# Kernel optimization log

Measured on AMD Instinct MI355X. Metric: run time of the kernel, lower is better.

## Reference

```python
import jax, jax.numpy as jnp
import numpy as np

MAX_ABS = 1.0          # assumed get_max_abs('T')
DT = 0.01              # forward default dt
TWO_PI = 2.0 * np.pi
B, D, N = 4096, 2048, 4096


def setup_inputs() -> dict:
    key = jax.random.key(0)
    k0, k1 = jax.random.split(key, 2)
    x = jax.random.normal(k0, (B, D), dtype=jnp.float32)
    # nn.Linear params
    W = jax.random.normal(k1, (N, D), dtype=jnp.float32) * (1.0 / np.sqrt(D))
    b = jnp.zeros((N,), dtype=jnp.float32)
    # oscillator params (as initialized in __init__)
    amplitude = jnp.ones((N,), dtype=jnp.float32)
    frequency = jnp.ones((N,), dtype=jnp.float32)
    phase_offset = jnp.zeros((N,), dtype=jnp.float32)
    damping = jnp.full((N,), 0.01, dtype=jnp.float32)
    return {"x": x, "W": W, "b": b, "amplitude": amplitude,
            "frequency": frequency, "phase_offset": phase_offset,
            "damping": damping}


def reference(x, W, b, amplitude, frequency, phase_offset, damping):
    # driving force: [B, N]
    force = x @ W.T + b
    omega_sq = (TWO_PI * frequency) ** 2  # [N]
    # t starts at 0 and is incremented ONCE per forward call
    t = DT

    def step(carry, f):
        state, vel = carry
        accel = -omega_sq * state - damping * vel + f
        vel = vel + accel * DT
        state = state + vel * DT
        return (state, vel), state

    init = (jnp.zeros((N,), x.dtype), jnp.zeros((N,), x.dtype))
    (_, _), states = jax.lax.scan(step, init, force)  # states: [B, N]

    # sinusoid term is identical for every batch step (t fixed within forward)
    osc = amplitude * jnp.sin(TWO_PI * frequency * t + phase_offset)  # [N]
    out = jnp.clip(states + osc, -MAX_ABS, MAX_ABS)
    return out
```

## Files before the change

### kernel.cpp

```cpp
#include <hip/hip_runtime.h>
#include <hip/hip_bf16.h>
#include <math.h>

#define MDIM 4096
#define KDIM 2048
#define NDIM 4096
#define DT   0.01f
#define TWO_PI_F 6.283185307179586f
#define CH 64
#define CL 64

typedef __attribute__((ext_vector_type(8))) short bf16x8;
typedef __attribute__((ext_vector_type(4))) float f32x4;

__device__ __forceinline__ unsigned short f2bf(float f) {
  unsigned int u = __float_as_uint(f);
  u += 0x7FFFu + ((u >> 16) & 1u);
  return (unsigned short)(u >> 16);
}
__device__ __forceinline__ float bf2f(unsigned short u) {
  return __uint_as_float(((unsigned int)u) << 16);
}

__global__ void cast_bf16_kernel(const float* __restrict__ src,
                                 unsigned short* __restrict__ dst, int n4) {
  int i = blockIdx.x * blockDim.x + threadIdx.x;
  if (i >= n4) return;
  float4 v = ((const float4*)src)[i];
  ushort4 o;
  o.x = f2bf(v.x); o.y = f2bf(v.y); o.z = f2bf(v.z); o.w = f2bf(v.w);
  ((ushort4*)dst)[i] = o;
}

__global__ __launch_bounds__(256, 2) void gemm_bt_kernel(
    const unsigned short* __restrict__ A,
    const unsigned short* __restrict__ Bm,
    const float* __restrict__ bias,
    unsigned short* __restrict__ C) {
  __shared__ __align__(16) unsigned short sA[128 * 32];
  __shared__ __align__(16) unsigned short sB[128 * 32];

  const int tid  = threadIdx.x;
  const int lane = tid & 63;
  const int wave = tid >> 6;
  const int wr = wave >> 1;
  const int wc = wave & 1;
  const int q  = lane >> 4;
  const int lm = lane & 15;

  const int bM = blockIdx.x * 128;
  const int bN = blockIdx.y * 128;

  f32x4 acc[4][4];
#pragma unroll
  for (int i = 0; i < 4; i++)
#pragma unroll
    for (int j = 0; j < 4; j++) acc[i][j] = (f32x4){0.f, 0.f, 0.f, 0.f};

  const int idx0 = tid;
  const int idx1 = tid + 256;
  const int r0 = idx0 >> 2, c0 = (idx0 & 3) * 8;
  const int r1 = idx1 >> 2, c1 = (idx1 & 3) * 8;

  for (int k0 = 0; k0 < KDIM; k0 += 32) {
    uint4 av0 = *(const uint4*)&A [(size_t)(bM + r0) * KDIM + k0 + c0];
    uint4 av1 = *(const uint4*)&A [(size_t)(bM + r1) * KDIM + k0 + c1];
    uint4 bv0 = *(const uint4*)&Bm[(size_t)(bN + r0) * KDIM + k0 + c0];
    uint4 bv1 = *(const uint4*)&Bm[(size_t)(bN + r1) * KDIM + k0 + c1];
    __syncthreads();
    *(uint4*)&sA[idx0 * 8] = av0;
    *(uint4*)&sA[idx1 * 8] = av1;
    *(uint4*)&sB[idx0 * 8] = bv0;
    *(uint4*)&sB[idx1 * 8] = bv1;
    __syncthreads();

    bf16x8 af[4], bfr[4];
#pragma unroll
    for (int mt = 0; mt < 4; mt++)
      af[mt]  = *(const bf16x8*)&sA[(wr * 64 + mt * 16 + lm) * 32 + q * 8];
#pragma unroll
    for (int nt = 0; nt < 4; nt++)
      bfr[nt] = *(const bf16x8*)&sB[(wc * 64 + nt * 16 + lm) * 32 + q * 8];

#pragma unroll
    for (int mt = 0; mt < 4; mt++)
#pragma unroll
      for (int nt = 0; nt < 4; nt++)
        acc[mt][nt] = __builtin_amdgcn_mfma_f32_16x16x32_bf16(
            af[mt], bfr[nt], acc[mt][nt], 0, 0, 0);
  }

#pragma unroll
  for (int nt = 0; nt < 4; nt++) {
    const int col = bN + wc * 64 + nt * 16 + lm;
    const float bz = bias[col];
#pragma unroll
    for (int mt = 0; mt < 4; mt++) {
      const int row0 = bM + wr * 64 + mt * 16 + q * 4;
#pragma unroll
      for (int r = 0; r < 4; r++)
        C[(size_t)(row0 + r) * NDIM + col] = f2bf(acc[mt][nt][r] + bz);
    }
  }
}

__global__ void scan_pass1(const unsigned short* __restrict__ force,
                           const float* __restrict__ freq,
                           const float* __restrict__ damp,
                           float* __restrict__ chunkS,
                           float* __restrict__ chunkV) {
  int gid = blockIdx.x * blockDim.x + threadIdx.x;
  int n = gid & (NDIM - 1);
  int c = gid >> 12;
  float om = TWO_PI_F * freq[n];
  float osq = om * om;
  float dp = damp[n];
  float s = 0.f, v = 0.f;
  const unsigned short* fp = force + (size_t)c * CL * NDIM + n;
#pragma unroll 8
  for (int i = 0; i < CL; i++) {
    float f = bf2f(fp[(size_t)i * NDIM]);
    float a = -osq * s - dp * v + f;
    v += a * DT;
    s += v * DT;
  }
  chunkS[gid] = s;
  chunkV[gid] = v;
}

__global__ void scan_pass2(const float* __restrict__ chunkS,
                           const float* __restrict__ chunkV,
                           const float* __restrict__ freq,
                           const float* __restrict__ damp,
                           float* __restrict__ carryS,
                           float* __restrict__ carryV) {
  int n = blockIdx.x * blockDim.x + threadIdx.x;
  float om = TWO_PI_F * freq[n];
  float osq = om * om;
  float dp = damp[n];
  float a00 = 1.f - osq * DT * DT, a01 = DT * (1.f - dp * DT);
  float a10 = -osq * DT,           a11 = 1.f - dp * DT;
#pragma unroll
  for (int i = 0; i < 6; i++) {
    float b00 = a00 * a00 + a01 * a10;
    float b01 = a00 * a01 + a01 * a11;
    float b10 = a10 * a00 + a11 * a10;
    float b11 = a10 * a01 + a11 * a11;
    a00 = b00; a01 = b01; a10 = b10; a11 = b11;
  }
  float cs = 0.f, cv = 0.f;
#pragma unroll 8
  for (int c = 0; c < CH; c++) {
    carryS[c * NDIM + n] = cs;
    carryV[c * NDIM + n] = cv;
    float ls = chunkS[c * NDIM + n];
    float lv = chunkV[c * NDIM + n];
    float ns = a00 * cs + a01 * cv + ls;
    float nv = a10 * cs + a11 * cv + lv;
    cs = ns; cv = nv;
  }
}

__global__ void scan_pass3(const unsigned short* __restrict__ force,
                           const float* __restrict__ amp,
                           const float* __restrict__ freq,
                           const float* __restrict__ phase,
                           const float* __restrict__ damp,
                           const float* __restrict__ carryS,
                           const float* __restrict__ carryV,
                           float* __restrict__ out) {
  int gid = blockIdx.x * blockDim.x + threadIdx.x;
  int n = gid & (NDIM - 1);
  int c = gid >> 12;
  float om = TWO_PI_F * freq[n];
  float osq = om * om;
  float dp = damp[n];
  float osc = amp[n] * sinf(om * DT + phase[n]);
  float s = carryS[gid], v = carryV[gid];
  const unsigned short* fp = force + (size_t)c * CL * NDIM + n;
  float* op = out + (size_t)c * CL * NDIM + n;
#pragma unroll 8
  for (int i = 0; i < CL; i++) {
    float f = bf2f(fp[(size_t)i * NDIM]);
    float a = -osq * s - dp * v + f;
    v += a * DT;
    s += v * DT;
    float o = s + osc;
    o = fminf(1.f, fmaxf(-1.f, o));
    op[(size_t)i * NDIM] = o;
  }
}

extern "C" void kernel_launch(void* const* d_in, const int* in_sizes, int n_in,
                              void* d_out, int out_size, void* d_ws, size_t ws_size,
                              hipStream_t stream) {
  const float* x     = (const float*)d_in[0];
  const float* W     = (const float*)d_in[1];
  const float* bias  = (const float*)d_in[2];
  const float* amp   = (const float*)d_in[3];
  const float* freq  = (const float*)d_in[4];
  const float* phase = (const float*)d_in[5];
  const float* damp  = (const float*)d_in[6];

  unsigned short* xbf   = (unsigned short*)d_ws;
  unsigned short* wbf   = xbf + (size_t)MDIM * KDIM;
  unsigned short* force = wbf + (size_t)NDIM * KDIM;
  float* chunkS = (float*)d_ws;
  float* chunkV = chunkS + CH * NDIM;
  float* carryS = chunkV + CH * NDIM;
  float* carryV = carryS + CH * NDIM;

  cast_bf16_kernel<<<(MDIM * KDIM / 4 + 255) / 256, 256, 0, stream>>>(
      x, xbf, MDIM * KDIM / 4);
  cast_bf16_kernel<<<(NDIM * KDIM / 4 + 255) / 256, 256, 0, stream>>>(
      W, wbf, NDIM * KDIM / 4);

  dim3 gg(MDIM / 128, NDIM / 128);
  gemm_bt_kernel<<<gg, 256, 0, stream>>>(xbf, wbf, bias, force);

  scan_pass1<<<CH * NDIM / 256, 256, 0, stream>>>(force, freq, damp,
                                                  chunkS, chunkV);
  scan_pass2<<<NDIM / 256, 256, 0, stream>>>(chunkS, chunkV, freq, damp,
                                             carryS, carryV);
  scan_pass3<<<CH * NDIM / 256, 256, 0, stream>>>(
      force, amp, freq, phase, damp, carryS, carryV, (float*)d_out);
}
```

Baseline: 235.3 us.

## Use direct global-to-LDS loads in GEMM, vectorize scans, merge cast kernels

```diff
diff --git a/kernel.cpp b/kernel.cpp
--- a/kernel.cpp
+++ b/kernel.cpp
@@ -13,6 +13,11 @@
 typedef __attribute__((ext_vector_type(8))) short bf16x8;
 typedef __attribute__((ext_vector_type(4))) float f32x4;
 
+#define GLD_LDS16(g, l)                                             \
+  __builtin_amdgcn_global_load_lds(                                 \
+      (const __attribute__((address_space(1))) unsigned int*)(g),   \
+      (__attribute__((address_space(3))) unsigned int*)(l), 16, 0, 0)
+
 __device__ __forceinline__ unsigned short f2bf(float f) {
   unsigned int u = __float_as_uint(f);
   u += 0x7FFFu + ((u >> 16) & 1u);
@@ -22,14 +27,21 @@
   return __uint_as_float(((unsigned int)u) << 16);
 }
 
-__global__ void cast_bf16_kernel(const float* __restrict__ src,
-                                 unsigned short* __restrict__ dst, int n4) {
+__global__ void cast2_bf16_kernel(const float* __restrict__ s0,
+                                  unsigned short* __restrict__ d0,
+                                  const float* __restrict__ s1,
+                                  unsigned short* __restrict__ d1,
+                                  int n4each) {
   int i = blockIdx.x * blockDim.x + threadIdx.x;
-  if (i >= n4) return;
-  float4 v = ((const float4*)src)[i];
+  const float4* sp;
+  ushort4* dp;
+  int j;
+  if (i < n4each) { sp = (const float4*)s0; dp = (ushort4*)d0; j = i; }
+  else            { sp = (const float4*)s1; dp = (ushort4*)d1; j = i - n4each; }
+  float4 v = sp[j];
   ushort4 o;
   o.x = f2bf(v.x); o.y = f2bf(v.y); o.z = f2bf(v.z); o.w = f2bf(v.w);
-  ((ushort4*)dst)[i] = o;
+  dp[j] = o;
 }
 
 __global__ __launch_bounds__(256, 2) void gemm_bt_kernel(
@@ -61,17 +73,17 @@
   const int idx1 = tid + 256;
   const int r0 = idx0 >> 2, c0 = (idx0 & 3) * 8;
   const int r1 = idx1 >> 2, c1 = (idx1 & 3) * 8;
+  const unsigned short* gA0 = A  + (size_t)(bM + r0) * KDIM + c0;
+  const unsigned short* gA1 = A  + (size_t)(bM + r1) * KDIM + c1;
+  const unsigned short* gB0 = Bm + (size_t)(bN + r0) * KDIM + c0;
+  const unsigned short* gB1 = Bm + (size_t)(bN + r1) * KDIM + c1;
 
   for (int k0 = 0; k0 < KDIM; k0 += 32) {
-    uint4 av0 = *(const uint4*)&A [(size_t)(bM + r0) * KDIM + k0 + c0];
-    uint4 av1 = *(const uint4*)&A [(size_t)(bM + r1) * KDIM + k0 + c1];
-    uint4 bv0 = *(const uint4*)&Bm[(size_t)(bN + r0) * KDIM + k0 + c0];
-    uint4 bv1 = *(const uint4*)&Bm[(size_t)(bN + r1) * KDIM + k0 + c1];
     __syncthreads();
-    *(uint4*)&sA[idx0 * 8] = av0;
-    *(uint4*)&sA[idx1 * 8] = av1;
-    *(uint4*)&sB[idx0 * 8] = bv0;
-    *(uint4*)&sB[idx1 * 8] = bv1;
+    GLD_LDS16(gA0 + k0, &sA[idx0 * 8]);
+    GLD_LDS16(gA1 + k0, &sA[idx1 * 8]);
+    GLD_LDS16(gB0 + k0, &sB[idx0 * 8]);
+    GLD_LDS16(gB1 + k0, &sB[idx1 * 8]);
     __syncthreads();
 
     bf16x8 af[4], bfr[4];
@@ -110,22 +122,30 @@
                            float* __restrict__ chunkS,
                            float* __restrict__ chunkV) {
   int gid = blockIdx.x * blockDim.x + threadIdx.x;
-  int n = gid & (NDIM - 1);
-  int c = gid >> 12;
-  float om = TWO_PI_F * freq[n];
-  float osq = om * om;
-  float dp = damp[n];
-  float s = 0.f, v = 0.f;
+  int n4 = gid & (NDIM / 4 - 1);
+  int c  = gid >> 10;
+  int n  = n4 * 4;
+  float4 fr = *(const float4*)&freq[n];
+  float4 dv = *(const float4*)&damp[n];
+  float osq[4] = {TWO_PI_F * fr.x, TWO_PI_F * fr.y, TWO_PI_F * fr.z, TWO_PI_F * fr.w};
+  float dp[4]  = {dv.x, dv.y, dv.z, dv.w};
+  float s[4] = {0.f, 0.f, 0.f, 0.f}, v[4] = {0.f, 0.f, 0.f, 0.f};
+#pragma unroll
+  for (int j = 0; j < 4; j++) osq[j] *= osq[j];
   const unsigned short* fp = force + (size_t)c * CL * NDIM + n;
-#pragma unroll 8
+#pragma unroll 4
   for (int i = 0; i < CL; i++) {
-    float f = bf2f(fp[(size_t)i * NDIM]);
-    float a = -osq * s - dp * v + f;
-    v += a * DT;
-    s += v * DT;
-  }
-  chunkS[gid] = s;
-  chunkV[gid] = v;
+    ushort4 fv = *(const ushort4*)&fp[(size_t)i * NDIM];
+    float f[4] = {bf2f(fv.x), bf2f(fv.y), bf2f(fv.z), bf2f(fv.w)};
+#pragma unroll
+    for (int j = 0; j < 4; j++) {
+      float a = -osq[j] * s[j] - dp[j] * v[j] + f[j];
+      v[j] += a * DT;
+      s[j] += v[j] * DT;
+    }
+  }
+  *(float4*)&chunkS[c * NDIM + n] = (float4){s[0], s[1], s[2], s[3]};
+  *(float4*)&chunkV[c * NDIM + n] = (float4){v[0], v[1], v[2], v[3]};
 }
 
 __global__ void scan_pass2(const float* __restrict__ chunkS,
@@ -170,24 +190,42 @@
                            const float* __restrict__ carryV,
                            float* __restrict__ out) {
   int gid = blockIdx.x * blockDim.x + threadIdx.x;
-  int n = gid & (NDIM - 1);
-  int c = gid >> 12;
-  float om = TWO_PI_F * freq[n];
-  float osq = om * om;
-  float dp = damp[n];
-  float osc = amp[n] * sinf(om * DT + phase[n]);
-  float s = carryS[gid], v = carryV[gid];
+  int n4 = gid & (NDIM / 4 - 1);
+  int c  = gid >> 10;
+  int n  = n4 * 4;
+  float4 fr = *(const float4*)&freq[n];
+  float4 dv = *(const float4*)&damp[n];
+  float4 am = *(const float4*)&amp[n];
+  float4 ph = *(const float4*)&phase[n];
+  float om[4] = {TWO_PI_F * fr.x, TWO_PI_F * fr.y, TWO_PI_F * fr.z, TWO_PI_F * fr.w};
+  float dp[4] = {dv.x, dv.y, dv.z, dv.w};
+  float osq[4], osc[4], s[4], v[4];
+  float amv[4] = {am.x, am.y, am.z, am.w};
+  float phv[4] = {ph.x, ph.y, ph.z, ph.w};
+#pragma unroll
+  for (int j = 0; j < 4; j++) {
+    osq[j] = om[j] * om[j];
+    osc[j] = amv[j] * sinf(om[j] * DT + phv[j]);
+  }
+  float4 csv = *(const float4*)&carryS[c * NDIM + n];
+  float4 cvv = *(const float4*)&carryV[c * NDIM + n];
+  s[0] = csv.x; s[1] = csv.y; s[2] = csv.z; s[3] = csv.w;
+  v[0] = cvv.x; v[1] = cvv.y; v[2] = cvv.z; v[3] = cvv.w;
   const unsigned short* fp = force + (size_t)c * CL * NDIM + n;
   float* op = out + (size_t)c * CL * NDIM + n;
-#pragma unroll 8
+#pragma unroll 4
   for (int i = 0; i < CL; i++) {
-    float f = bf2f(fp[(size_t)i * NDIM]);
-    float a = -osq * s - dp * v + f;
-    v += a * DT;
-    s += v * DT;
-    float o = s + osc;
-    o = fminf(1.f, fmaxf(-1.f, o));
-    op[(size_t)i * NDIM] = o;
+    ushort4 fv = *(const ushort4*)&fp[(size_t)i * NDIM];
+    float f[4] = {bf2f(fv.x), bf2f(fv.y), bf2f(fv.z), bf2f(fv.w)};
+    float o[4];
+#pragma unroll
+    for (int j = 0; j < 4; j++) {
+      float a = -osq[j] * s[j] - dp[j] * v[j] + f[j];
+      v[j] += a * DT;
+      s[j] += v[j] * DT;
+      o[j] = fminf(1.f, fmaxf(-1.f, s[j] + osc[j]));
+    }
+    *(float4*)&op[(size_t)i * NDIM] = (float4){o[0], o[1], o[2], o[3]};
   }
 }
 
@@ -210,18 +248,17 @@
   float* carryS = chunkV + CH * NDIM;
   float* carryV = carryS + CH * NDIM;
 
-  cast_bf16_kernel<<<(MDIM * KDIM / 4 + 255) / 256, 256, 0, stream>>>(
-      x, xbf, MDIM * KDIM / 4);
-  cast_bf16_kernel<<<(NDIM * KDIM / 4 + 255) / 256, 256, 0, stream>>>(
-      W, wbf, NDIM * KDIM / 4);
+  const int n4each = MDIM * KDIM / 4;
+  cast2_bf16_kernel<<<(2 * n4each + 255) / 256, 256, 0, stream>>>(
+      x, xbf, W, wbf, n4each);
 
   dim3 gg(MDIM / 128, NDIM / 128);
   gemm_bt_kernel<<<gg, 256, 0, stream>>>(xbf, wbf, bias, force);
 
-  scan_pass1<<<CH * NDIM / 256, 256, 0, stream>>>(force, freq, damp,
-                                                  chunkS, chunkV);
+  scan_pass1<<<CH * NDIM / 4 / 256, 256, 0, stream>>>(force, freq, damp,
+                                                      chunkS, chunkV);
   scan_pass2<<<NDIM / 256, 256, 0, stream>>>(chunkS, chunkV, freq, damp,
                                              carryS, carryV);
-  scan_pass3<<<CH * NDIM / 256, 256, 0, stream>>>(
+  scan_pass3<<<CH * NDIM / 4 / 256, 256, 0, stream>>>(
       force, amp, freq, phase, damp, carryS, carryV, (float*)d_out);
 }
```

After: 231.4 us. Within noise of the previous version (-1.6%).

## Fuse three-pass oscillator scan into one cooperative kernel with LDS-cached force

Applied to the files above, without the earlier changes.

```diff
diff --git a/kernel.cpp b/kernel.cpp
--- a/kernel.cpp
+++ b/kernel.cpp
@@ -1,6 +1,9 @@
 #include <hip/hip_runtime.h>
 #include <hip/hip_bf16.h>
+#include <hip/hip_cooperative_groups.h>
 #include <math.h>
+
+namespace cg = cooperative_groups;
 
 #define MDIM 4096
 #define KDIM 2048
@@ -22,14 +25,21 @@
   return __uint_as_float(((unsigned int)u) << 16);
 }
 
-__global__ void cast_bf16_kernel(const float* __restrict__ src,
-                                 unsigned short* __restrict__ dst, int n4) {
+__global__ void cast2_bf16_kernel(const float* __restrict__ s0,
+                                  unsigned short* __restrict__ d0,
+                                  const float* __restrict__ s1,
+                                  unsigned short* __restrict__ d1,
+                                  int n4each) {
   int i = blockIdx.x * blockDim.x + threadIdx.x;
-  if (i >= n4) return;
-  float4 v = ((const float4*)src)[i];
+  const float4* sp;
+  ushort4* dp;
+  int j;
+  if (i < n4each) { sp = (const float4*)s0; dp = (ushort4*)d0; j = i; }
+  else            { sp = (const float4*)s1; dp = (ushort4*)d1; j = i - n4each; }
+  float4 v = sp[j];
   ushort4 o;
   o.x = f2bf(v.x); o.y = f2bf(v.y); o.z = f2bf(v.z); o.w = f2bf(v.w);
-  ((ushort4*)dst)[i] = o;
+  dp[j] = o;
 }
 
 __global__ __launch_bounds__(256, 2) void gemm_bt_kernel(
@@ -104,90 +114,89 @@
   }
 }
 
-__global__ void scan_pass1(const unsigned short* __restrict__ force,
-                           const float* __restrict__ freq,
-                           const float* __restrict__ damp,
-                           float* __restrict__ chunkS,
-                           float* __restrict__ chunkV) {
-  int gid = blockIdx.x * blockDim.x + threadIdx.x;
-  int n = gid & (NDIM - 1);
-  int c = gid >> 12;
-  float om = TWO_PI_F * freq[n];
-  float osq = om * om;
-  float dp = damp[n];
-  float s = 0.f, v = 0.f;
-  const unsigned short* fp = force + (size_t)c * CL * NDIM + n;
+__global__ __launch_bounds__(256, 2) void scan_fused(
+    const unsigned short* __restrict__ force,
+    const float* __restrict__ amp,
+    const float* __restrict__ freq,
+    const float* __restrict__ phase,
+    const float* __restrict__ damp,
+    float* __restrict__ chunkS,
+    float* __restrict__ chunkV,
+    float* __restrict__ out) {
+  __shared__ __align__(16) unsigned short sF[CL * 512];
+
+  const int tid = threadIdx.x;
+  const int c = blockIdx.x >> 3;
+  const int colBase = (blockIdx.x & 7) * 512;
+
+#pragma unroll
+  for (int k = 0; k < 16; k++) {
+    int slot = tid + 256 * k;
+    *(uint4*)&sF[slot * 8] =
+        *(const uint4*)&force[((size_t)c * CL + (slot >> 6)) * NDIM +
+                              colBase + (slot & 63) * 8];
+  }
+  __syncthreads();
+
+  const int n = colBase + tid * 2;
+  float2 fr = *(const float2*)&freq[n];
+  float2 dv = *(const float2*)&damp[n];
+  const float om0 = TWO_PI_F * fr.x, om1 = TWO_PI_F * fr.y;
+  const float osq0 = om0 * om0,      osq1 = om1 * om1;
+  const float dp0 = dv.x,            dp1 = dv.y;
+
+  float s0 = 0.f, v0 = 0.f, s1 = 0.f, v1 = 0.f;
 #pragma unroll 8
   for (int i = 0; i < CL; i++) {
-    float f = bf2f(fp[(size_t)i * NDIM]);
-    float a = -osq * s - dp * v + f;
-    v += a * DT;
-    s += v * DT;
-  }
-  chunkS[gid] = s;
-  chunkV[gid] = v;
-}
-
-__global__ void scan_pass2(const float* __restrict__ chunkS,
-                           const float* __restrict__ chunkV,
-                           const float* __restrict__ freq,
-                           const float* __restrict__ damp,
-                           float* __restrict__ carryS,
-                           float* __restrict__ carryV) {
-  int n = blockIdx.x * blockDim.x + threadIdx.x;
-  float om = TWO_PI_F * freq[n];
-  float osq = om * om;
-  float dp = damp[n];
-  float a00 = 1.f - osq * DT * DT, a01 = DT * (1.f - dp * DT);
-  float a10 = -osq * DT,           a11 = 1.f - dp * DT;
+    ushort2 f2 = *(const ushort2*)&sF[i * 512 + tid * 2];
+    float f0 = bf2f(f2.x), f1 = bf2f(f2.y);
+    v0 += (-osq0 * s0 - dp0 * v0 + f0) * DT;  s0 += v0 * DT;
+    v1 += (-osq1 * s1 - dp1 * v1 + f1) * DT;  s1 += v1 * DT;
+  }
+  *(float2*)&chunkS[c * NDIM + n] = make_float2(s0, s1);
+  *(float2*)&chunkV[c * NDIM + n] = make_float2(v0, v1);
+  __threadfence();
+  cg::this_grid().sync();
+
+  float p00 = 1.f - osq0 * DT * DT, p01 = DT * (1.f - dp0 * DT);
+  float p10 = -osq0 * DT,           p11 = 1.f - dp0 * DT;
+  float q00 = 1.f - osq1 * DT * DT, q01 = DT * (1.f - dp1 * DT);
+  float q10 = -osq1 * DT,           q11 = 1.f - dp1 * DT;
 #pragma unroll
   for (int i = 0; i < 6; i++) {
-    float b00 = a00 * a00 + a01 * a10;
-    float b01 = a00 * a01 + a01 * a11;
-    float b10 = a10 * a00 + a11 * a10;
-    float b11 = a10 * a01 + a11 * a11;
-    a00 = b00; a01 = b01; a10 = b10; a11 = b11;
-  }
-  float cs = 0.f, cv = 0.f;
-#pragma unroll 8
-  for (int c = 0; c < CH; c++) {
-    carryS[c * NDIM + n] = cs;
-    carryV[c * NDIM + n] = cv;
-    float ls = chunkS[c * NDIM + n];
-    float lv = chunkV[c * NDIM + n];
-    float ns = a00 * cs + a01 * cv + ls;
-    float nv = a10 * cs + a11 * cv + lv;
-    cs = ns; cv = nv;
-  }
-}
-
-__global__ void scan_pass3(const unsigned short* __restrict__ force,
-                           const float* __restrict__ amp,
-                           const float* __restrict__ freq,
-                           const float* __restrict__ phase,
-                           const float* __restrict__ damp,
-                           const float* __restrict__ carryS,
-                           const float* __restrict__ carryV,
-                           float* __restrict__ out) {
-  int gid = blockIdx.x * blockDim.x + threadIdx.x;
-  int n = gid & (NDIM - 1);
-  int c = gid >> 12;
-  float om = TWO_PI_F * freq[n];
-  float osq = om * om;
-  float dp = damp[n];
-  float osc = amp[n] * sinf(om * DT + phase[n]);
-  float s = carryS[gid], v = carryV[gid];
-  const unsigned short* fp = force + (size_t)c * CL * NDIM + n;
-  float* op = out + (size_t)c * CL * NDIM + n;
+    float b00 = p00 * p00 + p01 * p10, b01 = p00 * p01 + p01 * p11;
+    float b10 = p10 * p00 + p11 * p10, b11 = p10 * p01 + p11 * p11;
+    p00 = b00; p01 = b01; p10 = b10; p11 = b11;
+    float d00 = q00 * q00 + q01 * q10, d01 = q00 * q01 + q01 * q11;
+    float d10 = q10 * q00 + q11 * q10, d11 = q10 * q01 + q11 * q11;
+    q00 = d00; q01 = d01; q10 = d10; q11 = d11;
+  }
+  float cs0 = 0.f, cv0 = 0.f, cs1 = 0.f, cv1 = 0.f;
+  for (int cc = 0; cc < c; cc++) {
+    float2 ls = *(const float2*)&chunkS[cc * NDIM + n];
+    float2 lv = *(const float2*)&chunkV[cc * NDIM + n];
+    float t0 = p00 * cs0 + p01 * cv0 + ls.x;
+    float u0 = p10 * cs0 + p11 * cv0 + lv.x;
+    cs0 = t0; cv0 = u0;
+    float t1 = q00 * cs1 + q01 * cv1 + ls.y;
+    float u1 = q10 * cs1 + q11 * cv1 + lv.y;
+    cs1 = t1; cv1 = u1;
+  }
+
+  float2 am = *(const float2*)&amp[n];
+  float2 ph = *(const float2*)&phase[n];
+  const float osc0 = am.x * sinf(om0 * DT + ph.x);
+  const float osc1 = am.y * sinf(om1 * DT + ph.y);
+  s0 = cs0; v0 = cv0; s1 = cs1; v1 = cv1;
 #pragma unroll 8
   for (int i = 0; i < CL; i++) {
-    float f = bf2f(fp[(size_t)i * NDIM]);
-    float a = -osq * s - dp * v + f;
-    v += a * DT;
-    s += v * DT;
-    float o = s + osc;
-    o = fminf(1.f, fmaxf(-1.f, o));
-    op[(size_t)i * NDIM] = o;
+    ushort2 f2 = *(const ushort2*)&sF[i * 512 + tid * 2];
+    float f0 = bf2f(f2.x), f1 = bf2f(f2.y);
+    v0 += (-osq0 * s0 - dp0 * v0 + f0) * DT;  s0 += v0 * DT;
+    v1 += (-osq1 * s1 - dp1 * v1 + f1) * DT;  s1 += v1 * DT;
+    float o0 = fminf(1.f, fmaxf(-1.f, s0 + osc0));
+    float o1 = fminf(1.f, fmaxf(-1.f, s1 + osc1));
+    *(float2*)&out[((size_t)c * CL + i) * NDIM + n] = make_float2(o0, o1);
   }
 }
 
@@ -207,21 +216,17 @@
   unsigned short* force = wbf + (size_t)NDIM * KDIM;
   float* chunkS = (float*)d_ws;
   float* chunkV = chunkS + CH * NDIM;
-  float* carryS = chunkV + CH * NDIM;
-  float* carryV = carryS + CH * NDIM;
-
-  cast_bf16_kernel<<<(MDIM * KDIM / 4 + 255) / 256, 256, 0, stream>>>(
-      x, xbf, MDIM * KDIM / 4);
-  cast_bf16_kernel<<<(NDIM * KDIM / 4 + 255) / 256, 256, 0, stream>>>(
-      W, wbf, NDIM * KDIM / 4);
+  float* outp   = (float*)d_out;
+
+  const int n4each = MDIM * KDIM / 4;
+  cast2_bf16_kernel<<<(2 * n4each + 255) / 256, 256, 0, stream>>>(
+      x, xbf, W, wbf, n4each);
 
   dim3 gg(MDIM / 128, NDIM / 128);
   gemm_bt_kernel<<<gg, 256, 0, stream>>>(xbf, wbf, bias, force);
 
-  scan_pass1<<<CH * NDIM / 256, 256, 0, stream>>>(force, freq, damp,
-                                                  chunkS, chunkV);
-  scan_pass2<<<NDIM / 256, 256, 0, stream>>>(chunkS, chunkV, freq, damp,
-                                             carryS, carryV);
-  scan_pass3<<<CH * NDIM / 256, 256, 0, stream>>>(
-      force, amp, freq, phase, damp, carryS, carryV, (float*)d_out);
-}
+  void* args[] = {(void*)&force, (void*)&amp, (void*)&freq, (void*)&phase,
+                  (void*)&damp, (void*)&chunkS, (void*)&chunkV, (void*)&outp};
+  hipLaunchCooperativeKernel((const void*)scan_fused, dim3(CH * 8), dim3(256),
+                             args, 0, stream);
+}
```

Result: slower. 326.7 us (+38.9%).

## Fuse bf16 cast and local chunk scan into GEMM, merge carry and output passes

Applied to the files above, without the earlier changes.

```diff
diff --git a/kernel.cpp b/kernel.cpp
--- a/kernel.cpp
+++ b/kernel.cpp
@@ -21,24 +21,23 @@
 __device__ __forceinline__ float bf2f(unsigned short u) {
   return __uint_as_float(((unsigned int)u) << 16);
 }
-
-__global__ void cast_bf16_kernel(const float* __restrict__ src,
-                                 unsigned short* __restrict__ dst, int n4) {
-  int i = blockIdx.x * blockDim.x + threadIdx.x;
-  if (i >= n4) return;
-  float4 v = ((const float4*)src)[i];
-  ushort4 o;
-  o.x = f2bf(v.x); o.y = f2bf(v.y); o.z = f2bf(v.z); o.w = f2bf(v.w);
-  ((ushort4*)dst)[i] = o;
-}
-
-__global__ __launch_bounds__(256, 2) void gemm_bt_kernel(
-    const unsigned short* __restrict__ A,
-    const unsigned short* __restrict__ Bm,
+__device__ __forceinline__ unsigned int pk2(float lo, float hi) {
+  __hip_bfloat162 h = __float22bfloat162_rn(make_float2(lo, hi));
+  return *(unsigned int*)&h;
+}
+
+__global__ __launch_bounds__(256, 2) void gemm_scan_kernel(
+    const float* __restrict__ A,
+    const float* __restrict__ Bm,
     const float* __restrict__ bias,
-    unsigned short* __restrict__ C) {
-  __shared__ __align__(16) unsigned short sA[128 * 32];
-  __shared__ __align__(16) unsigned short sB[128 * 32];
+    const float* __restrict__ freq,
+    const float* __restrict__ damp,
+    unsigned short* __restrict__ zpart,
+    float* __restrict__ chunkS,
+    float* __restrict__ chunkV) {
+  __shared__ __align__(16) unsigned short smem[16384];
+  unsigned short* sA = smem;
+  unsigned short* sB = smem + 4096;
 
   const int tid  = threadIdx.x;
   const int lane = tid & 63;
@@ -61,12 +60,24 @@
   const int idx1 = tid + 256;
   const int r0 = idx0 >> 2, c0 = (idx0 & 3) * 8;
   const int r1 = idx1 >> 2, c1 = (idx1 & 3) * 8;
+  const float* gA0 = A  + (size_t)(bM + r0) * KDIM + c0;
+  const float* gA1 = A  + (size_t)(bM + r1) * KDIM + c1;
+  const float* gB0 = Bm + (size_t)(bN + r0) * KDIM + c0;
+  const float* gB1 = Bm + (size_t)(bN + r1) * KDIM + c1;
 
   for (int k0 = 0; k0 < KDIM; k0 += 32) {
-    uint4 av0 = *(const uint4*)&A [(size_t)(bM + r0) * KDIM + k0 + c0];
-    uint4 av1 = *(const uint4*)&A [(size_t)(bM + r1) * KDIM + k0 + c1];
-    uint4 bv0 = *(const uint4*)&Bm[(size_t)(bN + r0) * KDIM + k0 + c0];
-    uint4 bv1 = *(const uint4*)&Bm[(size_t)(bN + r1) * KDIM + k0 + c1];
+    float4 aL0 = *(const float4*)(gA0 + k0);
+    float4 aH0 = *(const float4*)(gA0 + k0 + 4);
+    float4 aL1 = *(const float4*)(gA1 + k0);
+    float4 aH1 = *(const float4*)(gA1 + k0 + 4);
+    float4 bL0 = *(const float4*)(gB0 + k0);
+    float4 bH0 = *(const float4*)(gB0 + k0 + 4);
+    float4 bL1 = *(const float4*)(gB1 + k0);
+    float4 bH1 = *(const float4*)(gB1 + k0 + 4);
+    uint4 av0 = {pk2(aL0.x,aL0.y), pk2(aL0.z,aL0.w), pk2(aH0.x,aH0.y), pk2(aH0.z,aH0.w)};
+    uint4 av1 = {pk2(aL1.x,aL1.y), pk2(aL1.z,aL1.w), pk2(aH1.x,aH1.y), pk2(aH1.z,aH1.w)};
+    uint4 bv0 = {pk2(bL0.x,bL0.y), pk2(bL0.z,bL0.w), pk2(bH0.x,bH0.y), pk2(bH0.z,bH0.w)};
+    uint4 bv1 = {pk2(bL1.x,bL1.y), pk2(bL1.z,bL1.w), pk2(bH1.x,bH1.y), pk2(bH1.z,bH1.w)};
     __syncthreads();
     *(uint4*)&sA[idx0 * 8] = av0;
     *(uint4*)&sA[idx1 * 8] = av1;
@@ -90,104 +101,119 @@
             af[mt], bfr[nt], acc[mt][nt], 0, 0, 0);
   }
 
+  __syncthreads();
+  unsigned short* sT = smem + wave * 4096;
 #pragma unroll
   for (int nt = 0; nt < 4; nt++) {
-    const int col = bN + wc * 64 + nt * 16 + lm;
-    const float bz = bias[col];
-#pragma unroll
-    for (int mt = 0; mt < 4; mt++) {
-      const int row0 = bM + wr * 64 + mt * 16 + q * 4;
+    const float bz = bias[bN + wc * 64 + nt * 16 + lm];
+#pragma unroll
+    for (int mt = 0; mt < 4; mt++)
 #pragma unroll
       for (int r = 0; r < 4; r++)
-        C[(size_t)(row0 + r) * NDIM + col] = f2bf(acc[mt][nt][r] + bz);
-    }
-  }
-}
-
-__global__ void scan_pass1(const unsigned short* __restrict__ force,
-                           const float* __restrict__ freq,
-                           const float* __restrict__ damp,
-                           float* __restrict__ chunkS,
-                           float* __restrict__ chunkV) {
-  int gid = blockIdx.x * blockDim.x + threadIdx.x;
-  int n = gid & (NDIM - 1);
-  int c = gid >> 12;
-  float om = TWO_PI_F * freq[n];
-  float osq = om * om;
-  float dp = damp[n];
+        sT[(mt * 16 + q * 4 + r) * 64 + nt * 16 + lm] =
+            f2bf(acc[mt][nt][r] + bz);
+  }
+  __syncthreads();
+
+  const int gcol = bN + wc * 64 + lane;
+  const float om  = TWO_PI_F * freq[gcol];
+  const float osq = om * om;
+  const float dp  = damp[gcol];
   float s = 0.f, v = 0.f;
-  const unsigned short* fp = force + (size_t)c * CL * NDIM + n;
 #pragma unroll 8
   for (int i = 0; i < CL; i++) {
-    float f = bf2f(fp[(size_t)i * NDIM]);
-    float a = -osq * s - dp * v + f;
-    v += a * DT;
+    float f = bf2f(sT[i * 64 + lane]);
+    v += (-osq * s - dp * v + f) * DT;
     s += v * DT;
-  }
-  chunkS[gid] = s;
-  chunkV[gid] = v;
-}
-
-__global__ void scan_pass2(const float* __restrict__ chunkS,
-                           const float* __restrict__ chunkV,
-                           const float* __restrict__ freq,
-                           const float* __restrict__ damp,
-                           float* __restrict__ carryS,
-                           float* __restrict__ carryV) {
-  int n = blockIdx.x * blockDim.x + threadIdx.x;
-  float om = TWO_PI_F * freq[n];
-  float osq = om * om;
-  float dp = damp[n];
-  float a00 = 1.f - osq * DT * DT, a01 = DT * (1.f - dp * DT);
-  float a10 = -osq * DT,           a11 = 1.f - dp * DT;
-#pragma unroll
-  for (int i = 0; i < 6; i++) {
-    float b00 = a00 * a00 + a01 * a10;
-    float b01 = a00 * a01 + a01 * a11;
-    float b10 = a10 * a00 + a11 * a10;
-    float b11 = a10 * a01 + a11 * a11;
-    a00 = b00; a01 = b01; a10 = b10; a11 = b11;
-  }
-  float cs = 0.f, cv = 0.f;
-#pragma unroll 8
-  for (int c = 0; c < CH; c++) {
-    carryS[c * NDIM + n] = cs;
-    carryV[c * NDIM + n] = cv;
-    float ls = chunkS[c * NDIM + n];
-    float lv = chunkV[c * NDIM + n];
-    float ns = a00 * cs + a01 * cv + ls;
-    float nv = a10 * cs + a11 * cv + lv;
-    cs = ns; cv = nv;
-  }
-}
-
-__global__ void scan_pass3(const unsigned short* __restrict__ force,
-                           const float* __restrict__ amp,
-                           const float* __restrict__ freq,
-                           const float* __restrict__ phase,
-                           const float* __restrict__ damp,
-                           const float* __restrict__ carryS,
-                           const float* __restrict__ carryV,
-                           float* __restrict__ out) {
+    sT[i * 64 + lane] = f2bf(s);
+  }
+  const int chunk = 2 * blockIdx.x + wr;
+  chunkS[chunk * NDIM + gcol] = s;
+  chunkV[chunk * NDIM + gcol] = v;
+  __syncthreads();
+
+#pragma unroll
+  for (int k = 0; k < 8; k++) {
+    int slot = lane + 64 * k;
+    int row  = slot >> 3;
+    int col8 = (slot & 7) * 8;
+    *(uint4*)&zpart[(size_t)(bM + wr * 64 + row) * NDIM + bN + wc * 64 + col8] =
+        *(uint4*)&sT[row * 64 + col8];
+  }
+}
+
+__global__ void scan_out_kernel(const unsigned short* __restrict__ zpart,
+                                const float* __restrict__ amp,
+                                const float* __restrict__ freq,
+                                const float* __restrict__ phase,
+                                const float* __restrict__ damp,
+                                const float* __restrict__ chunkS,
+                                const float* __restrict__ chunkV,
+                                float* __restrict__ out) {
   int gid = blockIdx.x * blockDim.x + threadIdx.x;
-  int n = gid & (NDIM - 1);
-  int c = gid >> 12;
-  float om = TWO_PI_F * freq[n];
-  float osq = om * om;
-  float dp = damp[n];
-  float osc = amp[n] * sinf(om * DT + phase[n]);
-  float s = carryS[gid], v = carryV[gid];
-  const unsigned short* fp = force + (size_t)c * CL * NDIM + n;
+  int n4 = gid & (NDIM / 4 - 1);
+  int c  = gid >> 10;
+  int n  = n4 * 4;
+
+  float4 fr = *(const float4*)&freq[n];
+  float4 dv = *(const float4*)&damp[n];
+  float4 am = *(const float4*)&amp[n];
+  float4 ph = *(const float4*)&phase[n];
+  float omv[4] = {TWO_PI_F * fr.x, TWO_PI_F * fr.y, TWO_PI_F * fr.z, TWO_PI_F * fr.w};
+  float dpv[4] = {dv.x, dv.y, dv.z, dv.w};
+  float amv[4] = {am.x, am.y, am.z, am.w};
+  float phv[4] = {ph.x, ph.y, ph.z, ph.w};
+  float m00[4], m01[4], m10[4], m11[4];
+  float p00[4], p01[4], p10[4], p11[4];
+  float osc[4];
+#pragma unroll
+  for (int j = 0; j < 4; j++) {
+    float osq = omv[j] * omv[j];
+    m00[j] = 1.f - osq * DT * DT;  m01[j] = DT * (1.f - dpv[j] * DT);
+    m10[j] = -osq * DT;            m11[j] = 1.f - dpv[j] * DT;
+    p00[j] = m00[j]; p01[j] = m01[j]; p10[j] = m10[j]; p11[j] = m11[j];
+    osc[j] = amv[j] * sinf(omv[j] * DT + phv[j]);
+  }
+#pragma unroll
+  for (int i = 0; i < 6; i++)
+#pragma unroll
+    for (int j = 0; j < 4; j++) {
+      float b00 = p00[j] * p00[j] + p01[j] * p10[j];
+      float b01 = p00[j] * p01[j] + p01[j] * p11[j];
+      float b10 = p10[j] * p00[j] + p11[j] * p10[j];
+      float b11 = p10[j] * p01[j] + p11[j] * p11[j];
+      p00[j] = b00; p01[j] = b01; p10[j] = b10; p11[j] = b11;
+    }
+
+  float hs[4] = {0.f, 0.f, 0.f, 0.f}, hv[4] = {0.f, 0.f, 0.f, 0.f};
+  for (int cc = 0; cc < c; cc++) {
+    float4 ls = *(const float4*)&chunkS[cc * NDIM + n];
+    float4 lv = *(const float4*)&chunkV[cc * NDIM + n];
+    float lsv[4] = {ls.x, ls.y, ls.z, ls.w};
+    float lvv[4] = {lv.x, lv.y, lv.z, lv.w};
+#pragma unroll
+    for (int j = 0; j < 4; j++) {
+      float t = p00[j] * hs[j] + p01[j] * hv[j] + lsv[j];
+      float u = p10[j] * hs[j] + p11[j] * hv[j] + lvv[j];
+      hs[j] = t; hv[j] = u;
+    }
+  }
+
+  const unsigned short* zp = zpart + (size_t)c * CL * NDIM + n;
   float* op = out + (size_t)c * CL * NDIM + n;
-#pragma unroll 8
+#pragma unroll 4
   for (int i = 0; i < CL; i++) {
-    float f = bf2f(fp[(size_t)i * NDIM]);
-    float a = -osq * s - dp * v + f;
-    v += a * DT;
-    s += v * DT;
-    float o = s + osc;
-    o = fminf(1.f, fmaxf(-1.f, o));
-    op[(size_t)i * NDIM] = o;
+    ushort4 zv = *(const ushort4*)&zp[(size_t)i * NDIM];
+    float z[4] = {bf2f(zv.x), bf2f(zv.y), bf2f(zv.z), bf2f(zv.w)};
+    float o[4];
+#pragma unroll
+    for (int j = 0; j < 4; j++) {
+      float t = m00[j] * hs[j] + m01[j] * hv[j];
+      float u = m10[j] * hs[j] + m11[j] * hv[j];
+      hs[j] = t; hv[j] = u;
+      o[j] = fminf(1.f, fmaxf(-1.f, hs[j] + z[j] + osc[j]));
+    }
+    *(float4*)&op[(size_t)i * NDIM] = (float4){o[0], o[1], o[2], o[3]};
   }
 }
 
@@ -202,26 +228,14 @@
   const float* phase = (const float*)d_in[5];
   const float* damp  = (const float*)d_in[6];
 
-  unsigned short* xbf   = (unsigned short*)d_ws;
-  unsigned short* wbf   = xbf + (size_t)MDIM * KDIM;
-  unsigned short* force = wbf + (size_t)NDIM * KDIM;
-  float* chunkS = (float*)d_ws;
+  unsigned short* zpart = (unsigned short*)d_ws;
+  float* chunkS = (float*)((char*)d_ws + (size_t)MDIM * NDIM * 2);
   float* chunkV = chunkS + CH * NDIM;
-  float* carryS = chunkV + CH * NDIM;
-  float* carryV = carryS + CH * NDIM;
-
-  cast_bf16_kernel<<<(MDIM * KDIM / 4 + 255) / 256, 256, 0, stream>>>(
-      x, xbf, MDIM * KDIM / 4);
-  cast_bf16_kernel<<<(NDIM * KDIM / 4 + 255) / 256, 256, 0, stream>>>(
-      W, wbf, NDIM * KDIM / 4);
 
   dim3 gg(MDIM / 128, NDIM / 128);
-  gemm_bt_kernel<<<gg, 256, 0, stream>>>(xbf, wbf, bias, force);
-
-  scan_pass1<<<CH * NDIM / 256, 256, 0, stream>>>(force, freq, damp,
-                                                  chunkS, chunkV);
-  scan_pass2<<<NDIM / 256, 256, 0, stream>>>(chunkS, chunkV, freq, damp,
-                                             carryS, carryV);
-  scan_pass3<<<CH * NDIM / 256, 256, 0, stream>>>(
-      force, amp, freq, phase, damp, carryS, carryV, (float*)d_out);
-}
+  gemm_scan_kernel<<<gg, 256, 0, stream>>>(x, W, bias, freq, damp,
+                                           zpart, chunkS, chunkV);
+
+  scan_out_kernel<<<CH * NDIM / 4 / 256, 256, 0, stream>>>(
+      zpart, amp, freq, phase, damp, chunkS, chunkV, (float*)d_out);
+}
```

New measurement: 250.8 us. 1.07x slower.
